# Kernel optimization log

Hardware: AMD Instinct MI355X
Metric: run time of the kernel (lower is better)

## Reference

```python
import jax, jax.numpy as jnp
import numpy as np

N_NODES = 20000
N_EDGES = 100000
IN = 512
HID = 512
OUT = 512
EF = 128
NH = 16
HEAD = OUT // NH


def _ln(x):
    mu = jnp.mean(x, axis=-1, keepdims=True)
    var = jnp.var(x, axis=-1, keepdims=True)
    return (x - mu) / jnp.sqrt(var + 1e-5)


def _mlp(x, W1, b1, g, be, W2, b2):
    hdn = x @ W1 + b1
    hdn = _ln(hdn) * g + be
    hdn = jax.nn.relu(hdn)
    return hdn @ W2 + b2


def setup_inputs() -> dict:
    key = jax.random.key(0)
    ks = jax.random.split(key, 16)

    def w(k, i, o):
        return jax.random.normal(k, (i, o), jnp.float32) / np.float32(np.sqrt(i))

    inp = {
        'h': jax.random.normal(ks[0], (N_NODES, IN), jnp.float32),
        'edge_feat': jax.random.normal(ks[1], (N_EDGES, EF), jnp.float32),
        'edge_index': jax.random.randint(ks[2], (2, N_EDGES), 0, N_NODES, jnp.int32),
    }
    # hk / hv MLPs: kv_input_dim = IN + EF
    inp['hk_W1'] = w(ks[3], IN + EF, HID); inp['hk_b1'] = jnp.zeros((HID,), jnp.float32)
    inp['hk_g'] = jnp.ones((HID,), jnp.float32); inp['hk_be'] = jnp.zeros((HID,), jnp.float32)
    inp['hk_W2'] = w(ks[4], HID, OUT); inp['hk_b2'] = jnp.zeros((OUT,), jnp.float32)
    inp['hv_W1'] = w(ks[5], IN + EF, HID); inp['hv_b1'] = jnp.zeros((HID,), jnp.float32)
    inp['hv_g'] = jnp.ones((HID,), jnp.float32); inp['hv_be'] = jnp.zeros((HID,), jnp.float32)
    inp['hv_W2'] = w(ks[6], HID, OUT); inp['hv_b2'] = jnp.zeros((OUT,), jnp.float32)
    # hq MLP: input_dim -> output_dim
    inp['hq_W1'] = w(ks[7], IN, HID); inp['hq_b1'] = jnp.zeros((HID,), jnp.float32)
    inp['hq_g'] = jnp.ones((HID,), jnp.float32); inp['hq_be'] = jnp.zeros((HID,), jnp.float32)
    inp['hq_W2'] = w(ks[8], HID, OUT); inp['hq_b2'] = jnp.zeros((OUT,), jnp.float32)
    # node_output MLP: 2*hidden -> hidden
    inp['no_W1'] = w(ks[9], 2 * HID, HID); inp['no_b1'] = jnp.zeros((HID,), jnp.float32)
    inp['no_g'] = jnp.ones((HID,), jnp.float32); inp['no_be'] = jnp.zeros((HID,), jnp.float32)
    inp['no_W2'] = w(ks[10], HID, HID); inp['no_b2'] = jnp.zeros((HID,), jnp.float32)
    return inp


def reference(h, edge_feat, edge_index,
              hk_W1, hk_b1, hk_g, hk_be, hk_W2, hk_b2,
              hv_W1, hv_b1, hv_g, hv_be, hv_W2, hv_b2,
              hq_W1, hq_b1, hq_g, hq_be, hq_W2, hq_b2,
              no_W1, no_b1, no_g, no_be, no_W2, no_b2):
    N = h.shape[0]
    src, dst = edge_index[0], edge_index[1]
    # edge gather + per-edge K/V MLPs
    kv_in = jnp.concatenate([h[src], edge_feat], axis=-1)          # [E, IN+EF]
    k = _mlp(kv_in, hk_W1, hk_b1, hk_g, hk_be, hk_W2, hk_b2).reshape(-1, NH, HEAD)
    v = _mlp(kv_in, hv_W1, hv_b1, hv_g, hv_be, hv_W2, hv_b2).reshape(-1, NH, HEAD)
    q = _mlp(h, hq_W1, hq_b1, hq_g, hq_be, hq_W2, hq_b2).reshape(-1, NH, HEAD)
    # scatter softmax over incoming edges of each dst node
    logits = jnp.sum(q[dst] * k, axis=-1) / np.float32(np.sqrt(HEAD))  # [E, NH]
    mx = jax.ops.segment_max(logits, dst, num_segments=N)              # [N, NH]
    ex = jnp.exp(logits - mx[dst])
    den = jax.ops.segment_sum(ex, dst, num_segments=N)                 # [N, NH]
    alpha = ex / den[dst]                                              # [E, NH]
    # scatter-sum aggregate
    m = alpha[..., None] * v                                           # [E, NH, HEAD]
    out = jax.ops.segment_sum(m, dst, num_segments=N).reshape(N, OUT)
    out = _mlp(jnp.concatenate([out, h], axis=-1), no_W1, no_b1, no_g, no_be, no_W2, no_b2)
    return out + h
```

## Files before the change

### kernel.cpp

```cpp
#include <hip/hip_runtime.h>

#define NN 20000
#define NE 100000

typedef unsigned short u16;
typedef __bf16 bf16x8 __attribute__((ext_vector_type(8)));
typedef float f32x4 __attribute__((ext_vector_type(4)));
typedef short short8 __attribute__((ext_vector_type(8)));
typedef u16 u16x4 __attribute__((ext_vector_type(4)));

__device__ __forceinline__ float bf2f(u16 u) {
    union { unsigned int i; float f; } x; x.i = ((unsigned int)u) << 16; return x.f;
}
__device__ __forceinline__ u16 f2bf(float f) {
    union { float f; unsigned int i; } x; x.f = f;
    unsigned int r = x.i + 0x7FFFu + ((x.i >> 16) & 1u);
    return (u16)(r >> 16);
}

__device__ __forceinline__ void gl_lds16(const void* g, void* l) {
    __builtin_amdgcn_global_load_lds(
        (__attribute__((address_space(1))) const void*)g,
        (__attribute__((address_space(3))) void*)l, 16, 0, 0);
}

__global__ void cvt_k(const float* __restrict__ in, u16* __restrict__ out, long n) {
    long i = ((long)blockIdx.x * 256 + threadIdx.x) * 4;
    if (i < n) {
        f32x4 v = *(const f32x4*)(in + i);
        u16x4 o;
        #pragma unroll
        for (int j = 0; j < 4; j++) o[j] = f2bf(v[j]);
        *(u16x4*)(out + i) = o;
    }
}

__global__ __launch_bounds__(256)
void ttr_k(const float* __restrict__ W, u16* __restrict__ WT, int Kr) {
    __shared__ float tile[32][33];
    int k0 = blockIdx.x * 32, n0 = blockIdx.y * 32;
    int tx = threadIdx.x & 31, ty = threadIdx.x >> 5;
    #pragma unroll
    for (int i = 0; i < 4; i++)
        tile[ty + 8 * i][tx] = W[(size_t)(k0 + ty + 8 * i) * 512 + n0 + tx];
    __syncthreads();
    #pragma unroll
    for (int i = 0; i < 4; i++)
        WT[(size_t)(n0 + ty + 8 * i) * Kr + k0 + tx] = f2bf(tile[tx][ty + 8 * i]);
}

template<int AK, bool BIAS, bool RES, bool DEVM, bool OUTF, bool LOGIT>
__global__ __launch_bounds__(256, 2)
void gemm_k(const u16* __restrict__ A, const u16* __restrict__ A2,
            const int* __restrict__ eids, const int* __restrict__ Be, int ci, int cap,
            const u16* __restrict__ WT, const float* __restrict__ bias,
            const float* __restrict__ resid, void* __restrict__ Cv,
            const u16* __restrict__ qbv, const int* __restrict__ dstv, float* __restrict__ lgv,
            int Mh, int K, int Ast, int Cst)
{
    __shared__ u16 smem[128 * 128];
    u16* sA = smem;
    u16* sB = smem + 128 * 64;
    int M = Mh, b0 = 0;
    if constexpr (DEVM) {
        b0 = Be[ci];
        M = min(Be[ci + 1] - b0, cap);
    }
    const int m0 = blockIdx.x * 128;
    if (m0 >= M) return;
    const int t = threadIdx.x;
    const int n0 = blockIdx.y * 128;
    const int lane = t & 63;
    const int w = t >> 6;
    const int lrow = lane >> 3;
    const int swz = ((lane & 7) ^ lrow) * 8;
    const int ldst = w * 512 + lane * 8;

    size_t abase[4];
    #pragma unroll
    for (int p = 0; p < 4; p++) {
        int row = min(m0 + p * 32 + w * 8 + lrow, M - 1);
        if constexpr (AK == 3)      abase[p] = (size_t)eids[b0 + row] * 128;
        else if constexpr (AK == 2) abase[p] = (size_t)row * 512;
        else                        abase[p] = (size_t)row * Ast;
    }
    const int wm = w >> 1, wn = w & 1;
    const int lm = lane & 15, lk = lane >> 4;
    const int swzr = lm & 7;

    f32x4 acc[4][4] = {};

    for (int k0 = 0; k0 < K; k0 += 64) {
        #pragma unroll
        for (int p = 0; p < 4; p++) {
            const u16* g;
            if constexpr (AK == 2) {
                g = (k0 < 512) ? (A + abase[p] + k0 + swz) : (A2 + abase[p] + (k0 - 512) + swz);
            } else {
                g = A + abase[p] + k0 + swz;
            }
            gl_lds16(g, sA + p * 2048 + ldst);
        }
        #pragma unroll
        for (int p = 0; p < 4; p++)
            gl_lds16(WT + (size_t)(n0 + p * 32 + w * 8 + lrow) * K + k0 + swz, sB + p * 2048 + ldst);
        __syncthreads();

        bf16x8 av[2][4], bv[2][4];
        #pragma unroll
        for (int hf = 0; hf < 2; hf++) {
            #pragma unroll
            for (int mi = 0; mi < 4; mi++)
                av[hf][mi] = *(const bf16x8*)(sA + (wm * 64 + mi * 16 + lm) * 64 + (((hf * 4 + lk) ^ swzr) * 8));
            #pragma unroll
            for (int ni = 0; ni < 4; ni++)
                bv[hf][ni] = *(const bf16x8*)(sB + (wn * 64 + ni * 16 + lm) * 64 + (((hf * 4 + lk) ^ swzr) * 8));
        }
        #pragma unroll
        for (int hf = 0; hf < 2; hf++)
            #pragma unroll
            for (int mi = 0; mi < 4; mi++)
                #pragma unroll
                for (int ni = 0; ni < 4; ni++)
                    acc[mi][ni] = __builtin_amdgcn_mfma_f32_16x16x32_bf16(av[hf][mi], bv[hf][ni], acc[mi][ni], 0, 0, 0);
        __syncthreads();
    }

    float bvv[4];
    #pragma unroll
    for (int ni = 0; ni < 4; ni++) bvv[ni] = BIAS ? bias[n0 + wn * 64 + ni * 16 + lm] : 0.f;

    if constexpr (LOGIT) {
        const int qrow = t >> 4;
        const int qc = t & 15;
        #pragma unroll
        for (int p = 0; p < 8; p++) {
            int row = p * 16 + qrow;
            int grow = min(m0 + row, M - 1);
            int e = eids[b0 + grow];
            const u16* g = qbv + (size_t)dstv[e] * 512 + n0 + ((qc ^ (row & 7)) << 3);
            gl_lds16(g, smem + p * 2048 + t * 8);
        }
        __syncthreads();
        #pragma unroll
        for (int mi = 0; mi < 4; mi++) {
            #pragma unroll
            for (int r = 0; r < 4; r++) {
                int rloc = wm * 64 + mi * 16 + lk * 4 + r;
                float h0 = 0.f, h1 = 0.f;
                #pragma unroll
                for (int ni = 0; ni < 4; ni++) {
                    int cloc = wn * 64 + ni * 16 + lm;
                    int addr = rloc * 128 + ((((cloc >> 3) ^ (rloc & 7)) << 3) | (cloc & 7));
                    float qv = bf2f(smem[addr]);
                    float pr = (acc[mi][ni][r] + bvv[ni]) * qv;
                    if (ni < 2) h0 += pr; else h1 += pr;
                }
                #pragma unroll
                for (int o = 1; o < 16; o <<= 1) { h0 += __shfl_xor(h0, o); h1 += __shfl_xor(h1, o); }
                int grow = m0 + rloc;
                if (lm == 0 && grow < M) {
                    int hbase = (n0 >> 5) + wn * 2;
                    lgv[(size_t)(b0 + grow) * 16 + hbase]     = h0 * 0.17677669529663687f;
                    lgv[(size_t)(b0 + grow) * 16 + hbase + 1] = h1 * 0.17677669529663687f;
                }
            }
        }
        return;
    }

    #pragma unroll
    for (int mi = 0; mi < 4; mi++) {
        int rbase = m0 + wm * 64 + mi * 16 + lk * 4;
        #pragma unroll
        for (int ni = 0; ni < 4; ni++) {
            int n = n0 + wn * 64 + ni * 16 + lm;
            #pragma unroll
            for (int r = 0; r < 4; r++) {
                int row = rbase + r;
                if (row < M) {
                    float cv = acc[mi][ni][r] + bvv[ni];
                    if constexpr (RES) cv += resid[(size_t)row * 512 + n];
                    if constexpr (OUTF) ((float*)Cv)[(size_t)row * Cst + n] = cv;
                    else                ((u16*)Cv)[(size_t)row * Cst + n] = f2bf(cv);
                }
            }
        }
    }
}

template<int AK, bool BIAS, bool RES, bool OUTF>
__global__ __launch_bounds__(256, 3)
void gemmS_k(const u16* __restrict__ A, const u16* __restrict__ A2,
             const u16* __restrict__ WT, const float* __restrict__ bias,
             const float* __restrict__ resid, void* __restrict__ Cv,
             int M, int K, int Ast, int Cst)
{
    __shared__ u16 sA[64 * 64];
    __shared__ u16 sB[128 * 64];
    const int m0 = blockIdx.x * 64;
    if (m0 >= M) return;
    const int t = threadIdx.x;
    const int n0 = blockIdx.y * 128;
    const int lane = t & 63;
    const int w = t >> 6;
    const int lrow = lane >> 3;
    const int swz = ((lane & 7) ^ lrow) * 8;
    const int ldst = w * 512 + lane * 8;

    size_t abase[2];
    #pragma unroll
    for (int p = 0; p < 2; p++) {
        int row = min(m0 + p * 32 + w * 8 + lrow, M - 1);
        if constexpr (AK == 2) abase[p] = (size_t)row * 512;
        else                   abase[p] = (size_t)row * Ast;
    }
    const int wm = w >> 1, wn = w & 1;
    const int lm = lane & 15, lk = lane >> 4;
    const int swzr = lm & 7;

    f32x4 acc[2][4] = {};

    for (int k0 = 0; k0 < K; k0 += 64) {
        #pragma unroll
        for (int p = 0; p < 2; p++) {
            const u16* g;
            if constexpr (AK == 2) {
                g = (k0 < 512) ? (A + abase[p] + k0 + swz) : (A2 + abase[p] + (k0 - 512) + swz);
            } else {
                g = A + abase[p] + k0 + swz;
            }
            gl_lds16(g, sA + p * 2048 + ldst);
        }
        #pragma unroll
        for (int p = 0; p < 4; p++)
            gl_lds16(WT + (size_t)(n0 + p * 32 + w * 8 + lrow) * K + k0 + swz, sB + p * 2048 + ldst);
        __syncthreads();

        bf16x8 av[2][2], bv[2][4];
        #pragma unroll
        for (int hf = 0; hf < 2; hf++) {
            #pragma unroll
            for (int mi = 0; mi < 2; mi++)
                av[hf][mi] = *(const bf16x8*)(sA + (wm * 32 + mi * 16 + lm) * 64 + (((hf * 4 + lk) ^ swzr) * 8));
            #pragma unroll
            for (int ni = 0; ni < 4; ni++)
                bv[hf][ni] = *(const bf16x8*)(sB + (wn * 64 + ni * 16 + lm) * 64 + (((hf * 4 + lk) ^ swzr) * 8));
        }
        #pragma unroll
        for (int hf = 0; hf < 2; hf++)
            #pragma unroll
            for (int mi = 0; mi < 2; mi++)
                #pragma unroll
                for (int ni = 0; ni < 4; ni++)
                    acc[mi][ni] = __builtin_amdgcn_mfma_f32_16x16x32_bf16(av[hf][mi], bv[hf][ni], acc[mi][ni], 0, 0, 0);
        __syncthreads();
    }

    float bvv[4];
    #pragma unroll
    for (int ni = 0; ni < 4; ni++) bvv[ni] = BIAS ? bias[n0 + wn * 64 + ni * 16 + lm] : 0.f;
    #pragma unroll
    for (int mi = 0; mi < 2; mi++) {
        int rbase = m0 + wm * 32 + mi * 16 + lk * 4;
        #pragma unroll
        for (int ni = 0; ni < 4; ni++) {
            int n = n0 + wn * 64 + ni * 16 + lm;
            #pragma unroll
            for (int r = 0; r < 4; r++) {
                int row = rbase + r;
                if (row < M) {
                    float cv = acc[mi][ni][r] + bvv[ni];
                    if constexpr (RES) cv += resid[(size_t)row * 512 + n];
                    if constexpr (OUTF) ((float*)Cv)[(size_t)row * Cst + n] = cv;
                    else                ((u16*)Cv)[(size_t)row * Cst + n] = f2bf(cv);
                }
            }
        }
    }
}

template<bool GATHER, bool DEVM>
__global__ __launch_bounds__(256)
void ln_relu_k(u16* __restrict__ hid, int hst, const u16* __restrict__ gsrc, int gst,
               const int* __restrict__ eids, const int* __restrict__ srcv,
               const float* __restrict__ b1, const float* __restrict__ g, const float* __restrict__ be,
               int Mh, const int* __restrict__ Be, int ci, int cap) {
    int M = Mh, b0 = 0;
    if constexpr (DEVM) { b0 = Be[ci]; M = min(Be[ci + 1] - Be[ci], cap); }
    int wid = threadIdx.x >> 6, lane = threadIdx.x & 63;
    long r = (long)blockIdx.x * 4 + wid;
    if (r >= M) return;
    u16* p = hid + r * hst + lane * 8;
    short8 v = *(const short8*)p;
    float x[8]; float s = 0.f, s2 = 0.f;
    if constexpr (GATHER) {
        int eid = eids[b0 + r];
        const u16* gp = gsrc + (size_t)srcv[eid] * gst + lane * 8;
        short8 gv = *(const short8*)gp;
        #pragma unroll
        for (int j = 0; j < 8; j++) x[j] = bf2f((u16)v[j]) + bf2f((u16)gv[j]) + b1[lane * 8 + j];
    } else {
        #pragma unroll
        for (int j = 0; j < 8; j++) x[j] = bf2f((u16)v[j]) + b1[lane * 8 + j];
    }
    #pragma unroll
    for (int j = 0; j < 8; j++) { s += x[j]; s2 += x[j] * x[j]; }
    #pragma unroll
    for (int o = 32; o > 0; o >>= 1) { s += __shfl_xor(s, o); s2 += __shfl_xor(s2, o); }
    float mu = s * (1.f / 512.f);
    float inv = rsqrtf(s2 * (1.f / 512.f) - mu * mu + 1e-5f);
    short8 ov;
    #pragma unroll
    for (int j = 0; j < 8; j++) {
        float y = (x[j] - mu) * inv * g[lane * 8 + j] + be[lane * 8 + j];
        ov[j] = (short)f2bf(fmaxf(y, 0.f));
    }
    *(short8*)p = ov;
}

__global__ void zero_k(int* a, int n) { int i = blockIdx.x * 256 + threadIdx.x; if (i < n) a[i] = 0; }
__global__ void count_k(const int* __restrict__ dst, int* __restrict__ counts) {
    int i = blockIdx.x * 256 + threadIdx.x;
    if (i < NE) atomicAdd(&counts[dst[i]], 1);
}
__global__ __launch_bounds__(1024)
void scan_k(const int* __restrict__ counts, int* __restrict__ offs) {
    __shared__ int part[1024];
    int t = threadIdx.x;
    const int chunk = (NN + 1023) / 1024;
    int lo = t * chunk; if (lo > NN) lo = NN;
    int hi = lo + chunk; if (hi > NN) hi = NN;
    int s = 0;
    for (int i = lo; i < hi; i++) s += counts[i];
    part[t] = s;
    __syncthreads();
    for (int o = 1; o < 1024; o <<= 1) {
        int v2 = 0;
        if (t >= o) v2 = part[t - o];
        __syncthreads();
        part[t] += v2;
        __syncthreads();
    }
    int base = (t > 0) ? part[t - 1] : 0;
    for (int i = lo; i < hi; i++) { offs[i] = base; base += counts[i]; }
    if (t == 1023) offs[NN] = part[1023];
}
__global__ void scatter_k(const int* __restrict__ dst, const int* __restrict__ offs,
                          int* __restrict__ cur, int* __restrict__ eids) {
    int i = blockIdx.x * 256 + threadIdx.x;
    if (i < NE) {
        int d = dst[i];
        int pos = atomicAdd(&cur[d], 1);
        eids[offs[d] + pos] = i;
    }
}
__global__ void bounds_k(const int* __restrict__ offs, int* __restrict__ Pn, int* __restrict__ Be,
                         int NC, int CEt) {
    int c = threadIdx.x;
    if (c > NC) return;
    int n;
    if (c == 0) n = 0;
    else if (c == NC) n = NN;
    else {
        int target = c * CEt;
        int lo = 0, hi = NN;
        while (lo < hi) { int mid = (lo + hi + 1) >> 1; if (offs[mid] <= target) lo = mid; else hi = mid - 1; }
        n = lo;
    }
    Pn[c] = n; Be[c] = offs[n];
}

__global__ __launch_bounds__(256)
void mxden_k(const float* __restrict__ lg, const int* __restrict__ offs,
             float* __restrict__ mx, float* __restrict__ den) {
    int wid = threadIdx.x >> 6, lane = threadIdx.x & 63;
    int n = blockIdx.x * 4 + wid;
    if (n >= NN) return;
    int lo = offs[n], hi = offs[n + 1];
    int head = lane & 15, j = lane >> 4;
    float m = -1e30f;
    for (int pe = lo + j; pe < hi; pe += 4)
        m = fmaxf(m, lg[(long)pe * 16 + head]);
    m = fmaxf(m, __shfl_xor(m, 16));
    m = fmaxf(m, __shfl_xor(m, 32));
    float d = 0.f;
    for (int pe = lo + j; pe < hi; pe += 4)
        d += __expf(lg[(long)pe * 16 + head] - m);
    d += __shfl_xor(d, 16);
    d += __shfl_xor(d, 32);
    if (j == 0) { mx[n * 16 + head] = m; den[n * 16 + head] = d; }
}

__global__ __launch_bounds__(256)
void aggc_k(const float* __restrict__ lg, const u16* __restrict__ v,
            const int* __restrict__ offs, const float* __restrict__ mx, const float* __restrict__ den,
            const int* __restrict__ Pn, const int* __restrict__ Be, int ci, int cap,
            u16* __restrict__ agg) {
    int wid = threadIdx.x >> 6, lane = threadIdx.x & 63;
    int n = blockIdx.x * 4 + wid;
    if (n >= NN) return;
    if (n < Pn[ci] || n >= Pn[ci + 1]) return;
    int lo = offs[n], hi = offs[n + 1], b0 = Be[ci];
    int head = lane >> 2;
    float m = mx[n * 16 + head];
    float dv = den[n * 16 + head];
    float rn = (hi > lo) ? (1.f / dv) : 0.f;
    float acc[8] = {0, 0, 0, 0, 0, 0, 0, 0};
    for (int pe = lo; pe < hi; pe++) {
        int r = pe - b0;
        if (r >= cap) break;
        float wgt = __expf(lg[(long)pe * 16 + head] - m);
        short8 vv = *(const short8*)(v + (long)r * 512 + lane * 8);
        #pragma unroll
        for (int j = 0; j < 8; j++) acc[j] += wgt * bf2f((u16)vv[j]);
    }
    short8 ov;
    #pragma unroll
    for (int j = 0; j < 8; j++) ov[j] = (short)f2bf(acc[j] * rn);
    *(short8*)(agg + (long)n * 512 + lane * 8) = ov;
}

extern "C" void kernel_launch(void* const* d_in, const int* in_sizes, int n_in,
                              void* d_out, int out_size, void* d_ws, size_t ws_size,
                              hipStream_t stream) {
    const float* h     = (const float*)d_in[0];
    const float* efeat = (const float*)d_in[1];
    const int*   eidx  = (const int*)d_in[2];
    const int* src = eidx;
    const int* dst = eidx + NE;
    const float* hkW1 = (const float*)d_in[3];  const float* hkb1 = (const float*)d_in[4];
    const float* hkg  = (const float*)d_in[5];  const float* hkbe = (const float*)d_in[6];
    const float* hkW2 = (const float*)d_in[7];  const float* hkb2 = (const float*)d_in[8];
    const float* hvW1 = (const float*)d_in[9];  const float* hvb1 = (const float*)d_in[10];
    const float* hvg  = (const float*)d_in[11]; const float* hvbe = (const float*)d_in[12];
    const float* hvW2 = (const float*)d_in[13]; const float* hvb2 = (const float*)d_in[14];
    const float* hqW1 = (const float*)d_in[15]; const float* hqb1 = (const float*)d_in[16];
    const float* hqg  = (const float*)d_in[17]; const float* hqbe = (const float*)d_in[18];
    const float* hqW2 = (const float*)d_in[19]; const float* hqb2 = (const float*)d_in[20];
    const float* noW1 = (const float*)d_in[21]; const float* nob1 = (const float*)d_in[22];
    const float* nog  = (const float*)d_in[23]; const float* nobe = (const float*)d_in[24];
    const float* noW2 = (const float*)d_in[25]; const float* nob2 = (const float*)d_in[26];
    (void)in_sizes; (void)n_in; (void)out_size;

    char* wsp = (char*)d_ws;
    auto take = [&](size_t b) -> char* {
        char* r = wsp; wsp += (b + 255) & ~(size_t)255; return r;
    };
    u16* hb    = (u16*)take((size_t)NN * 512 * 2);
    u16* efb   = (u16*)take((size_t)NE * 128 * 2);
    u16* qb    = (u16*)take((size_t)NN * 512 * 2);
    u16* aggb  = (u16*)take((size_t)NN * 512 * 2);
    u16* NP    = (u16*)take((size_t)NN * 1536 * 2);
    float* lgb = (float*)take((size_t)NE * 16 * 4);
    float* mxb = (float*)take((size_t)NN * 16 * 4);
    float* denb= (float*)take((size_t)NN * 16 * 4);
    u16* WTn    = (u16*)take((size_t)1536 * 512 * 2);
    u16* noW1T  = (u16*)take(512 * 1024 * 2);
    u16* hkW1Te = (u16*)take(512 * 128 * 2);
    u16* hvW1Te = (u16*)take(512 * 128 * 2);
    u16* hkW2T  = (u16*)take(512 * 512 * 2);
    u16* hvW2T  = (u16*)take(512 * 512 * 2);
    u16* hqW2T  = (u16*)take(512 * 512 * 2);
    u16* noW2T  = (u16*)take(512 * 512 * 2);
    int* counts = (int*)take(NN * 4);
    int* offs   = (int*)take((NN + 1) * 4);
    int* cur    = (int*)take(NN * 4);
    int* eids   = (int*)take(NE * 4);
    int* Pn     = (int*)take(64 * 4);
    int* Bed    = (int*)take(64 * 4);

    size_t base = (size_t)(wsp - (char*)d_ws);
    const int ncs[15] = {1, 2, 3, 4, 5, 6, 8, 10, 13, 16, 20, 25, 32, 40, 50};
    int NC = 50;
    size_t cap = (size_t)((NE + 49) / 50) + 2048;
    for (int i = 0; i < 15; i++) {
        int nc = ncs[i];
        int cet = (NE + nc - 1) / nc;
        size_t c2 = (nc == 1) ? (size_t)NE : (size_t)cet + 2048;
        size_t buf = (c2 * 1024 + 255) & ~(size_t)255;
        if (base + 2 * buf <= ws_size) { NC = nc; cap = c2; break; }
    }
    size_t chunkbuf = (cap * 1024 + 255) & ~(size_t)255;
    u16* hidC = (u16*)take(chunkbuf);
    u16* kvC  = (u16*)take(chunkbuf);
    const int icap = (int)cap;
    const int CEt = (NE + NC - 1) / NC;

    cvt_k<<<((NN * 512 / 4) + 255) / 256, 256, 0, stream>>>(h, hb, (long)NN * 512);
    cvt_k<<<((NE * 128 / 4) + 255) / 256, 256, 0, stream>>>(efeat, efb, (long)NE * 128);

    dim3 tb(256);
    ttr_k<<<dim3(16, 16), tb, 0, stream>>>(hqW1, WTn, 512);
    ttr_k<<<dim3(16, 16), tb, 0, stream>>>(hkW1, WTn + 512 * 512, 512);
    ttr_k<<<dim3(16, 16), tb, 0, stream>>>(hvW1, WTn + 2 * 512 * 512, 512);
    ttr_k<<<dim3(4, 16),  tb, 0, stream>>>(hkW1 + 512 * 512, hkW1Te, 128);
    ttr_k<<<dim3(4, 16),  tb, 0, stream>>>(hvW1 + 512 * 512, hvW1Te, 128);
    ttr_k<<<dim3(32, 16), tb, 0, stream>>>(noW1, noW1T, 1024);
    ttr_k<<<dim3(16, 16), tb, 0, stream>>>(hkW2, hkW2T, 512);
    ttr_k<<<dim3(16, 16), tb, 0, stream>>>(hvW2, hvW2T, 512);
    ttr_k<<<dim3(16, 16), tb, 0, stream>>>(hqW2, hqW2T, 512);
    ttr_k<<<dim3(16, 16), tb, 0, stream>>>(noW2, noW2T, 512);

    zero_k<<<(NN + 255) / 256, 256, 0, stream>>>(counts, NN);
    zero_k<<<(NN + 255) / 256, 256, 0, stream>>>(cur, NN);
    count_k<<<(NE + 255) / 256, 256, 0, stream>>>(dst, counts);
    scan_k<<<1, 1024, 0, stream>>>(counts, offs);
    scatter_k<<<(NE + 255) / 256, 256, 0, stream>>>(dst, offs, cur, eids);
    bounds_k<<<1, 64, 0, stream>>>(offs, Pn, Bed, NC, CEt);

    dim3 gNP((NN + 127) / 128, 12);
    dim3 gNS((NN + 63) / 64, 4);
    dim3 gC(((int)cap + 127) / 128, 4);
    int lnN = (NN + 3) / 4;
    int lnC = ((int)cap + 3) / 4;

    gemm_k<0, false, false, false, false, false><<<gNP, 256, 0, stream>>>(
        hb, nullptr, nullptr, nullptr, 0, 0, WTn, nullptr, nullptr, NP,
        nullptr, nullptr, nullptr, NN, 512, 512, 1536);

    ln_relu_k<false, false><<<lnN, 256, 0, stream>>>(NP, 1536, nullptr, 0, nullptr, nullptr,
                                                     hqb1, hqg, hqbe, NN, nullptr, 0, 0);
    gemmS_k<0, true, false, false><<<gNS, 256, 0, stream>>>(NP, nullptr, hqW2T, hqb2, nullptr, qb,
                                                            NN, 512, 1536, 512);

    for (int c = 0; c < NC; c++) {
        gemm_k<3, false, false, true, false, false><<<gC, 256, 0, stream>>>(
            efb, nullptr, eids, Bed, c, icap, hkW1Te, nullptr, nullptr, hidC,
            nullptr, nullptr, nullptr, 0, 128, 128, 512);
        ln_relu_k<true, true><<<lnC, 256, 0, stream>>>(hidC, 512, NP + 512, 1536, eids, src,
                                                       hkb1, hkg, hkbe, 0, Bed, c, icap);
        gemm_k<0, true, false, true, false, true><<<gC, 256, 0, stream>>>(
            hidC, nullptr, eids, Bed, c, icap, hkW2T, hkb2, nullptr, nullptr,
            qb, dst, lgb, 0, 512, 512, 512);
    }

    mxden_k<<<lnN, 256, 0, stream>>>(lgb, offs, mxb, denb);

    for (int c = 0; c < NC; c++) {
        gemm_k<3, false, false, true, false, false><<<gC, 256, 0, stream>>>(
            efb, nullptr, eids, Bed, c, icap, hvW1Te, nullptr, nullptr, hidC,
            nullptr, nullptr, nullptr, 0, 128, 128, 512);
        ln_relu_k<true, true><<<lnC, 256, 0, stream>>>(hidC, 512, NP + 1024, 1536, eids, src,
                                                       hvb1, hvg, hvbe, 0, Bed, c, icap);
        gemm_k<0, true, false, true, false, false><<<gC, 256, 0, stream>>>(
            hidC, nullptr, nullptr, Bed, c, icap, hvW2T, hvb2, nullptr, kvC,
            nullptr, nullptr, nullptr, 0, 512, 512, 512);
        aggc_k<<<lnN, 256, 0, stream>>>(lgb, kvC, offs, mxb, denb, Pn, Bed, c, icap, aggb);
    }

    gemmS_k<2, false, false, false><<<gNS, 256, 0, stream>>>(aggb, hb, noW1T, nullptr, nullptr, qb,
                                                             NN, 1024, 512, 512);
    ln_relu_k<false, false><<<lnN, 256, 0, stream>>>(qb, 512, nullptr, 0, nullptr, nullptr,
                                                     nob1, nog, nobe, NN, nullptr, 0, 0);
    gemmS_k<0, true, true, true><<<gNS, 256, 0, stream>>>(qb, nullptr, noW2T, nob2, h, d_out,
                                                          NN, 512, 512, 512);
}
```

Baseline: 744.9 us.

## Fuse edge-feature GEMM with gathered LayerNorm-ReLU and swap grid axes

Adds a g1ln_k kernel that computes the per-edge edge-feature GEMM (K=128) for a 32-row tile and applies the gathered node-projection add, bias, LayerNorm and ReLU in the epilogue through an LDS staging buffer. This replaces a separate GEMM plus ln_relu pass and removes the bf16 round trip of the hidden activations between them. GEMM grids are transposed so the N tiles vary fastest, letting blocks that share an A row-tile run together for better cache reuse. The final residual now reads bf16 h instead of fp32, which halves that read but adds rounding error to the output.

```diff
diff --git a/kernel.cpp b/kernel.cpp
--- a/kernel.cpp
+++ b/kernel.cpp
@@ -49,12 +49,12 @@
         WT[(size_t)(n0 + ty + 8 * i) * Kr + k0 + tx] = f2bf(tile[tx][ty + 8 * i]);
 }
 
-template<int AK, bool BIAS, bool RES, bool DEVM, bool OUTF, bool LOGIT>
+template<int AK, bool BIAS, bool DEVM, bool OUTF, bool LOGIT>
 __global__ __launch_bounds__(256, 2)
 void gemm_k(const u16* __restrict__ A, const u16* __restrict__ A2,
             const int* __restrict__ eids, const int* __restrict__ Be, int ci, int cap,
             const u16* __restrict__ WT, const float* __restrict__ bias,
-            const float* __restrict__ resid, void* __restrict__ Cv,
+            void* __restrict__ Cv,
             const u16* __restrict__ qbv, const int* __restrict__ dstv, float* __restrict__ lgv,
             int Mh, int K, int Ast, int Cst)
 {
@@ -66,10 +66,10 @@
         b0 = Be[ci];
         M = min(Be[ci + 1] - b0, cap);
     }
-    const int m0 = blockIdx.x * 128;
+    const int m0 = blockIdx.y * 128;
     if (m0 >= M) return;
     const int t = threadIdx.x;
-    const int n0 = blockIdx.y * 128;
+    const int n0 = blockIdx.x * 128;
     const int lane = t & 63;
     const int w = t >> 6;
     const int lrow = lane >> 3;
@@ -80,9 +80,8 @@
     #pragma unroll
     for (int p = 0; p < 4; p++) {
         int row = min(m0 + p * 32 + w * 8 + lrow, M - 1);
-        if constexpr (AK == 3)      abase[p] = (size_t)eids[b0 + row] * 128;
-        else if constexpr (AK == 2) abase[p] = (size_t)row * 512;
-        else                        abase[p] = (size_t)row * Ast;
+        if constexpr (AK == 2) abase[p] = (size_t)row * 512;
+        else                   abase[p] = (size_t)row * Ast;
     }
     const int wm = w >> 1, wn = w & 1;
     const int lm = lane & 15, lk = lane >> 4;
@@ -180,7 +179,6 @@
                 int row = rbase + r;
                 if (row < M) {
                     float cv = acc[mi][ni][r] + bvv[ni];
-                    if constexpr (RES) cv += resid[(size_t)row * 512 + n];
                     if constexpr (OUTF) ((float*)Cv)[(size_t)row * Cst + n] = cv;
                     else                ((u16*)Cv)[(size_t)row * Cst + n] = f2bf(cv);
                 }
@@ -189,7 +187,7 @@
     }
 }
 
-template<int AK, bool BIAS, bool RES, bool OUTF>
+template<int AK, bool BIAS, bool RES, bool OUTF, bool RESB>
 __global__ __launch_bounds__(256, 3)
 void gemmS_k(const u16* __restrict__ A, const u16* __restrict__ A2,
              const u16* __restrict__ WT, const float* __restrict__ bias,
@@ -198,10 +196,10 @@
 {
     __shared__ u16 sA[64 * 64];
     __shared__ u16 sB[128 * 64];
-    const int m0 = blockIdx.x * 64;
+    const int m0 = blockIdx.y * 64;
     if (m0 >= M) return;
     const int t = threadIdx.x;
-    const int n0 = blockIdx.y * 128;
+    const int n0 = blockIdx.x * 128;
     const int lane = t & 63;
     const int w = t >> 6;
     const int lrow = lane >> 3;
@@ -271,7 +269,10 @@
                 int row = rbase + r;
                 if (row < M) {
                     float cv = acc[mi][ni][r] + bvv[ni];
-                    if constexpr (RES) cv += resid[(size_t)row * 512 + n];
+                    if constexpr (RES) {
+                        if constexpr (RESB) cv += bf2f(((const u16*)resid)[(size_t)row * 512 + n]);
+                        else                cv += resid[(size_t)row * 512 + n];
+                    }
                     if constexpr (OUTF) ((float*)Cv)[(size_t)row * Cst + n] = cv;
                     else                ((u16*)Cv)[(size_t)row * Cst + n] = f2bf(cv);
                 }
@@ -280,30 +281,129 @@
     }
 }
 
-template<bool GATHER, bool DEVM>
+__global__ __launch_bounds__(256, 2)
+void g1ln_k(const u16* __restrict__ efb, const u16* __restrict__ WTe,
+            const u16* __restrict__ NPp, const int* __restrict__ eids, const int* __restrict__ srcv,
+            const int* __restrict__ Be, int ci, int cap,
+            const float* __restrict__ b1, const float* __restrict__ g, const float* __restrict__ be,
+            u16* __restrict__ outb)
+{
+    __shared__ u16 lds[4096 + 16384];
+    u16* sA = lds;
+    u16* sB = lds + 4096;
+    float* sC = (float*)(lds + 4096);
+    int b0 = Be[ci];
+    int M = min(Be[ci + 1] - b0, cap);
+    const int m0 = blockIdx.x * 32;
+    if (m0 >= M) return;
+    const int t = threadIdx.x;
+    const int lane = t & 63;
+    const int w = t >> 6;
+    const int lm = lane & 15, lk = lane >> 4;
+
+    #pragma unroll
+    for (int p = 0; p < 2; p++) {
+        int slot = p * 256 + t;
+        int row = slot >> 4, gph = slot & 15;
+        int gsrc = (gph & 8) | ((gph & 7) ^ (row & 7));
+        int eid = eids[b0 + min(m0 + row, M - 1)];
+        gl_lds16(efb + (size_t)eid * 128 + gsrc * 8, sA + slot * 8);
+    }
+
+    f32x4 acc[2][8] = {};
+    for (int ks = 0; ks < 4; ks++) {
+        #pragma unroll
+        for (int p = 0; p < 8; p++) {
+            int slot = p * 256 + t;
+            int n = slot >> 2, cph = slot & 3;
+            int csrc = cph ^ (n & 3);
+            gl_lds16(WTe + (size_t)n * 128 + ks * 32 + csrc * 8, sB + slot * 8);
+        }
+        __syncthreads();
+        bf16x8 av[2], bv[8];
+        #pragma unroll
+        for (int mi = 0; mi < 2; mi++) {
+            int row = mi * 16 + lm;
+            int gl = ks * 4 + lk;
+            int gph = (gl & 8) | ((gl & 7) ^ (row & 7));
+            av[mi] = *(const bf16x8*)(sA + row * 128 + gph * 8);
+        }
+        #pragma unroll
+        for (int ni = 0; ni < 8; ni++) {
+            int n = w * 128 + ni * 16 + lm;
+            int cph = lk ^ (n & 3);
+            bv[ni] = *(const bf16x8*)(sB + n * 32 + cph * 8);
+        }
+        #pragma unroll
+        for (int mi = 0; mi < 2; mi++)
+            #pragma unroll
+            for (int ni = 0; ni < 8; ni++)
+                acc[mi][ni] = __builtin_amdgcn_mfma_f32_16x16x32_bf16(av[mi], bv[ni], acc[mi][ni], 0, 0, 0);
+        __syncthreads();
+    }
+
+    for (int half = 0; half < 2; half++) {
+        #pragma unroll
+        for (int ni = 0; ni < 8; ni++) {
+            int col = w * 128 + ni * 16 + lm;
+            int c4 = col >> 2;
+            #pragma unroll
+            for (int r = 0; r < 4; r++) {
+                int row_l = lk * 4 + r;
+                int ph4 = (c4 & ~7) | ((c4 & 7) ^ (row_l & 7));
+                sC[row_l * 512 + ph4 * 4 + (col & 3)] = acc[half][ni][r];
+            }
+        }
+        __syncthreads();
+        #pragma unroll
+        for (int i = 0; i < 4; i++) {
+            int row_l = w * 4 + i;
+            int row_g = m0 + half * 16 + row_l;
+            if (row_g < M) {
+                int g0 = lane * 2, g1 = g0 + 1;
+                int p0 = (g0 & ~7) | ((g0 & 7) ^ (row_l & 7));
+                int p1 = (g1 & ~7) | ((g1 & 7) ^ (row_l & 7));
+                f32x4 ca = *(const f32x4*)(sC + row_l * 512 + p0 * 4);
+                f32x4 cb = *(const f32x4*)(sC + row_l * 512 + p1 * 4);
+                int eid = eids[b0 + row_g];
+                const u16* gp = NPp + (size_t)srcv[eid] * 1536 + lane * 8;
+                short8 gv = *(const short8*)gp;
+                float x[8]; float s = 0.f, s2 = 0.f;
+                #pragma unroll
+                for (int j = 0; j < 4; j++) x[j] = ca[j] + bf2f((u16)gv[j]) + b1[lane * 8 + j];
+                #pragma unroll
+                for (int j = 4; j < 8; j++) x[j] = cb[j - 4] + bf2f((u16)gv[j]) + b1[lane * 8 + j];
+                #pragma unroll
+                for (int j = 0; j < 8; j++) { s += x[j]; s2 += x[j] * x[j]; }
+                #pragma unroll
+                for (int o = 32; o > 0; o >>= 1) { s += __shfl_xor(s, o); s2 += __shfl_xor(s2, o); }
+                float mu = s * (1.f / 512.f);
+                float inv = rsqrtf(s2 * (1.f / 512.f) - mu * mu + 1e-5f);
+                short8 ov;
+                #pragma unroll
+                for (int j = 0; j < 8; j++) {
+                    float y = (x[j] - mu) * inv * g[lane * 8 + j] + be[lane * 8 + j];
+                    ov[j] = (short)f2bf(fmaxf(y, 0.f));
+                }
+                *(short8*)(outb + (size_t)row_g * 512 + lane * 8) = ov;
+            }
+        }
+        __syncthreads();
+    }
+}
+
 __global__ __launch_bounds__(256)
-void ln_relu_k(u16* __restrict__ hid, int hst, const u16* __restrict__ gsrc, int gst,
-               const int* __restrict__ eids, const int* __restrict__ srcv,
+void ln_relu_k(u16* __restrict__ hid, int hst,
                const float* __restrict__ b1, const float* __restrict__ g, const float* __restrict__ be,
-               int Mh, const int* __restrict__ Be, int ci, int cap) {
-    int M = Mh, b0 = 0;
-    if constexpr (DEVM) { b0 = Be[ci]; M = min(Be[ci + 1] - Be[ci], cap); }
+               int M) {
     int wid = threadIdx.x >> 6, lane = threadIdx.x & 63;
     long r = (long)blockIdx.x * 4 + wid;
     if (r >= M) return;
     u16* p = hid + r * hst + lane * 8;
     short8 v = *(const short8*)p;
     float x[8]; float s = 0.f, s2 = 0.f;
-    if constexpr (GATHER) {
-        int eid = eids[b0 + r];
-        const u16* gp = gsrc + (size_t)srcv[eid] * gst + lane * 8;
-        short8 gv = *(const short8*)gp;
-        #pragma unroll
-        for (int j = 0; j < 8; j++) x[j] = bf2f((u16)v[j]) + bf2f((u16)gv[j]) + b1[lane * 8 + j];
-    } else {
-        #pragma unroll
-        for (int j = 0; j < 8; j++) x[j] = bf2f((u16)v[j]) + b1[lane * 8 + j];
-    }
+    #pragma unroll
+    for (int j = 0; j < 8; j++) x[j] = bf2f((u16)v[j]) + b1[lane * 8 + j];
     #pragma unroll
     for (int j = 0; j < 8; j++) { s += x[j]; s2 += x[j] * x[j]; }
     #pragma unroll
@@ -509,50 +609,42 @@
     scatter_k<<<(NE + 255) / 256, 256, 0, stream>>>(dst, offs, cur, eids);
     bounds_k<<<1, 64, 0, stream>>>(offs, Pn, Bed, NC, CEt);
 
-    dim3 gNP((NN + 127) / 128, 12);
-    dim3 gNS((NN + 63) / 64, 4);
-    dim3 gC(((int)cap + 127) / 128, 4);
+    dim3 gNP(12, (NN + 127) / 128);
+    dim3 gNS(4, (NN + 63) / 64);
+    dim3 gC(4, ((int)cap + 127) / 128);
     int lnN = (NN + 3) / 4;
-    int lnC = ((int)cap + 3) / 4;
-
-    gemm_k<0, false, false, false, false, false><<<gNP, 256, 0, stream>>>(
-        hb, nullptr, nullptr, nullptr, 0, 0, WTn, nullptr, nullptr, NP,
+    int g1b = ((int)cap + 31) / 32;
+
+    gemm_k<0, false, false, false, false><<<gNP, 256, 0, stream>>>(
+        hb, nullptr, nullptr, nullptr, 0, 0, WTn, nullptr, NP,
         nullptr, nullptr, nullptr, NN, 512, 512, 1536);
 
-    ln_relu_k<false, false><<<lnN, 256, 0, stream>>>(NP, 1536, nullptr, 0, nullptr, nullptr,
-                                                     hqb1, hqg, hqbe, NN, nullptr, 0, 0);
-    gemmS_k<0, true, false, false><<<gNS, 256, 0, stream>>>(NP, nullptr, hqW2T, hqb2, nullptr, qb,
-                                                            NN, 512, 1536, 512);
+    ln_relu_k<<<lnN, 256, 0, stream>>>(NP, 1536, hqb1, hqg, hqbe, NN);
+    gemmS_k<0, true, false, false, false><<<gNS, 256, 0, stream>>>(NP, nullptr, hqW2T, hqb2, nullptr, qb,
+                                                                   NN, 512, 1536, 512);
 
     for (int c = 0; c < NC; c++) {
-        gemm_k<3, false, false, true, false, false><<<gC, 256, 0, stream>>>(
-            efb, nullptr, eids, Bed, c, icap, hkW1Te, nullptr, nullptr, hidC,
-            nullptr, nullptr, nullptr, 0, 128, 128, 512);
-        ln_relu_k<true, true><<<lnC, 256, 0, stream>>>(hidC, 512, NP + 512, 1536, eids, src,
-                                                       hkb1, hkg, hkbe, 0, Bed, c, icap);
-        gemm_k<0, true, false, true, false, true><<<gC, 256, 0, stream>>>(
-            hidC, nullptr, eids, Bed, c, icap, hkW2T, hkb2, nullptr, nullptr,
+        g1ln_k<<<g1b, 256, 0, stream>>>(efb, hkW1Te, NP + 512, eids, src, Bed, c, icap,
+                                        hkb1, hkg, hkbe, hidC);
+        gemm_k<0, true, true, false, true><<<gC, 256, 0, stream>>>(
+            hidC, nullptr, eids, Bed, c, icap, hkW2T, hkb2, nullptr,
             qb, dst, lgb, 0, 512, 512, 512);
     }
 
     mxden_k<<<lnN, 256, 0, stream>>>(lgb, offs, mxb, denb);
 
     for (int c = 0; c < NC; c++) {
-        gemm_k<3, false, false, true, false, false><<<gC, 256, 0, stream>>>(
-            efb, nullptr, eids, Bed, c, icap, hvW1Te, nullptr, nullptr, hidC,
-            nullptr, nullptr, nullptr, 0, 128, 128, 512);
-        ln_relu_k<true, true><<<lnC, 256, 0, stream>>>(hidC, 512, NP + 1024, 1536, eids, src,
-                                                       hvb1, hvg, hvbe, 0, Bed, c, icap);
-        gemm_k<0, true, false, true, false, false><<<gC, 256, 0, stream>>>(
-            hidC, nullptr, nullptr, Bed, c, icap, hvW2T, hvb2, nullptr, kvC,
+        g1ln_k<<<g1b, 256, 0, stream>>>(efb, hvW1Te, NP + 1024, eids, src, Bed, c, icap,
+                                        hvb1, hvg, hvbe, hidC);
+        gemm_k<0, true, true, false, false><<<gC, 256, 0, stream>>>(
+            hidC, nullptr, nullptr, Bed, c, icap, hvW2T, hvb2, kvC,
             nullptr, nullptr, nullptr, 0, 512, 512, 512);
         aggc_k<<<lnN, 256, 0, stream>>>(lgb, kvC, offs, mxb, denb, Pn, Bed, c, icap, aggb);
     }
 
-    gemmS_k<2, false, false, false><<<gNS, 256, 0, stream>>>(aggb, hb, noW1T, nullptr, nullptr, qb,
-                                                             NN, 1024, 512, 512);
-    ln_relu_k<false, false><<<lnN, 256, 0, stream>>>(qb, 512, nullptr, 0, nullptr, nullptr,
-                                                     nob1, nog, nobe, NN, nullptr, 0, 0);
-    gemmS_k<0, true, true, true><<<gNS, 256, 0, stream>>>(qb, nullptr, noW2T, nob2, h, d_out,
-                                                          NN, 512, 512, 512);
-}
+    gemmS_k<2, false, false, false, false><<<gNS, 256, 0, stream>>>(aggb, hb, noW1T, nullptr, nullptr, qb,
+                                                                    NN, 1024, 512, 512);
+    ln_relu_k<<<lnN, 256, 0, stream>>>(qb, 512, nob1, nog, nobe, NN);
+    gemmS_k<0, true, true, true, true><<<gNS, 256, 0, stream>>>(qb, nullptr, noW2T, nob2, (const float*)hb, d_out,
+                                                                NN, 512, 512, 512);
+}
```

After: 749.8 us. Within noise of the previous version (+0.7%).
